# Kernel optimization log

Hardware: AMD Instinct MI355X
Metric: run time of the kernel (lower is better)

## Reference

```python
import jax, jax.numpy as jnp
import numpy as np

NB, H = 4, 8          # blocks, heads
B, S = 2, 1024        # batch, seq
D, HID = 512, 512     # input_dim, hidden_dim (must match, see zeros_like(x) branch)
# mod computed from neurochem BEFORE _modulate_neurochem, using init values
MOD = 0.5 * 1.1 + 0.5 * 0.7 + 0.5 * 1.3 - 0.0 * 1.2  # = 1.55


def setup_inputs() -> dict:
    key = jax.random.key(0)
    ks = jax.random.split(key, 12)
    sc = 1.0 / np.sqrt(D)
    inp = {
        "x": jax.random.normal(ks[0], (B, S, D), jnp.float32),
        "Wq": jax.random.normal(ks[1], (NB, D, HID), jnp.float32) * sc,
        "bq": jax.random.normal(ks[2], (NB, HID), jnp.float32) * sc,
        "Wk": jax.random.normal(ks[3], (NB, D, HID), jnp.float32) * sc,
        "bk": jax.random.normal(ks[4], (NB, HID), jnp.float32) * sc,
        "Wv": jax.random.normal(ks[5], (NB, D, HID), jnp.float32) * sc,
        "bv": jax.random.normal(ks[6], (NB, HID), jnp.float32) * sc,
        "Wo": jax.random.normal(ks[7], (NB, HID, D), jnp.float32) * sc,
        "bo": jax.random.normal(ks[8], (NB, D), jnp.float32) * sc,
        "strength": jax.random.uniform(ks[9], (NB, H, H), jnp.float32),
        # gate = (osc_mask * spike_mask > 0.5) materialized as 0/1 floats
        "gate": (jax.random.uniform(ks[10], (NB, H)) < 0.7).astype(jnp.float32),
    }
    return inp


def reference(x, Wq, bq, Wk, bk, Wv, bv, Wo, bo, strength, gate):
    # per-block projections (shared across heads in the original loop)
    q = jnp.einsum('bsd,ndh->nbsh', x, Wq) + bq[:, None, None, :]
    k = jnp.einsum('bsd,ndh->nbsh', x, Wk) + bk[:, None, None, :]
    v = jnp.einsum('bsd,ndh->nbsh', x, Wv) + bv[:, None, None, :]
    scores = jnp.einsum('nbsh,nbth->nbst', q, k) / jnp.sqrt(jnp.float32(HID))
    # per-head scalar bias: diagonal synaptic strength, clamped
    s = jnp.clip(jnp.diagonal(strength, axis1=1, axis2=2), 0.01, 1.0)  # [NB, H]
    scaled = scores[:, None] * s[:, :, None, None, None]  # [NB, H, B, S, S]
    probs = jax.nn.softmax(scaled, axis=-1)
    # head outputs summed with the 0/1 osc*spike gate
    head_sum = jnp.einsum('nhbst,nbtd,nh->nbsd', probs, v, gate)  # [NB, B, S, HID]
    block_out = jnp.einsum('nbsd,ndo->nbso', head_sum, Wo) + bo[:, None, None, :]
    return block_out.sum(axis=0) * jnp.float32(MOD)
```

## Files before the change

kernel.cpp:

```cpp
#include <hip/hip_runtime.h>
#include <math.h>

#define NBLK   4
#define NH     8
#define BATCH  2
#define SEQ    1024
#define DIM    512
#define HIDDEN 512
#define MODF   1.55f
#define INV_SQRT_HID 0.04419417382415922f

typedef __bf16 bf16;
typedef __bf16 bf16x4 __attribute__((ext_vector_type(4)));
typedef __bf16 bf16x8 __attribute__((ext_vector_type(8)));
typedef float  floatx4 __attribute__((ext_vector_type(4)));

constexpr int BM = 128, BN = 128, BK = 32;

__device__ __forceinline__ void load16_lds(const bf16* g, bf16* l) {
    __builtin_amdgcn_global_load_lds(
        (__attribute__((address_space(1))) void*)g,
        (__attribute__((address_space(3))) void*)l, 16, 0, 0);
}

__device__ __forceinline__ void stage32(
    const bf16* __restrict__ Ab, int lda,
    const bf16* __restrict__ Bb, int ldb, int k0,
    bf16* As, bf16* Bs, int w, int l)
{
    const int s0 = 2 * w, s1 = s0 + 1;
    const int r0 = s0 * 16 + (l >> 2);
    const int r1 = s1 * 16 + (l >> 2);
    const int kc = (l & 3) * 8;
    load16_lds(Ab + (size_t)r0 * lda + k0 + kc, As + s0 * 512);
    load16_lds(Ab + (size_t)r1 * lda + k0 + kc, As + s1 * 512);
    load16_lds(Bb + (size_t)r0 * ldb + k0 + kc, Bs + s0 * 512);
    load16_lds(Bb + (size_t)r1 * ldb + k0 + kc, Bs + s1 * 512);
}

__device__ __forceinline__ void comp32(
    const bf16* As, const bf16* Bs,
    int wr, int wc, int fr, int fk, floatx4 (&acc)[4][4])
{
    bf16x8 af[4], bg[4];
#pragma unroll
    for (int i = 0; i < 4; ++i)
        af[i] = *(const bf16x8*)&As[(wr + i * 16 + fr) * BK + fk];
#pragma unroll
    for (int j = 0; j < 4; ++j)
        bg[j] = *(const bf16x8*)&Bs[(wc + j * 16 + fr) * BK + fk];
#pragma unroll
    for (int i = 0; i < 4; ++i)
#pragma unroll
        for (int j = 0; j < 4; ++j)
            acc[i][j] = __builtin_amdgcn_mfma_f32_16x16x32_bf16(
                af[i], bg[j], acc[i][j], 0, 0, 0);
}

__device__ __forceinline__ void mfma_nt(
    const bf16* __restrict__ A, int lda,
    const bf16* __restrict__ B, int ldb,
    int K, int m0, int n0, floatx4 (&acc)[4][4])
{
    __shared__ __align__(16) bf16 As0[BM * BK];
    __shared__ __align__(16) bf16 Bs0[BN * BK];
    __shared__ __align__(16) bf16 As1[BM * BK];
    __shared__ __align__(16) bf16 Bs1[BN * BK];

    const int tid = threadIdx.x;
    const int l   = tid & 63;
    const int w   = tid >> 6;
    const int wr  = (w >> 1) * 64;
    const int wc  = (w & 1) * 64;
    const int fr  = l & 15;
    const int fk  = (l >> 4) * 8;

    const bf16* Ab = A + (size_t)m0 * lda;
    const bf16* Bb = B + (size_t)n0 * ldb;

    const int nIter = K / BK;
    stage32(Ab, lda, Bb, ldb, 0, As0, Bs0, w, l);
    for (int k = 0; k < nIter; k += 2) {
        __syncthreads();
        if (k + 1 < nIter)
            stage32(Ab, lda, Bb, ldb, (k + 1) * BK, As1, Bs1, w, l);
        comp32(As0, Bs0, wr, wc, fr, fk, acc);
        __syncthreads();
        if (k + 2 < nIter)
            stage32(Ab, lda, Bb, ldb, (k + 2) * BK, As0, Bs0, w, l);
        comp32(As1, Bs1, wr, wc, fr, fk, acc);
    }
}

__global__ __launch_bounds__(256) void xconv_kernel(
    const float* __restrict__ x, bf16* __restrict__ xb)
{
    const int t = blockIdx.x * 256 + threadIdx.x;
    const float4 v = ((const float4*)x)[t];
    bf16x4 o = { (bf16)v.x, (bf16)v.y, (bf16)v.z, (bf16)v.w };
    *(bf16x4*)&xb[(size_t)t * 4] = o;
}

__global__ __launch_bounds__(256) void transpose_w_kernel(
    const float* __restrict__ Wq, const float* __restrict__ Wk,
    const float* __restrict__ Wv, const float* __restrict__ Wo,
    bf16* __restrict__ WqT, bf16* __restrict__ WkT,
    bf16* __restrict__ WvT, bf16* __restrict__ WoT)
{
    __shared__ float tile[32][33];
    const int z = blockIdx.z;
    const int mat = z >> 2, n = z & 3;
    const float* src; bf16* dst;
    if (mat == 0)      { src = Wq; dst = WqT; }
    else if (mat == 1) { src = Wk; dst = WkT; }
    else if (mat == 2) { src = Wv; dst = WvT; }
    else               { src = Wo; dst = WoT; }
    src += (size_t)n * 512 * 512;
    dst += (size_t)n * 512 * 512;

    const int tx = threadIdx.x & 31, ty = threadIdx.x >> 5;
    const int x0 = blockIdx.x * 32, y0 = blockIdx.y * 32;
#pragma unroll
    for (int r = 0; r < 4; ++r)
        tile[ty + r * 8][tx] = src[(size_t)(y0 + ty + r * 8) * 512 + x0 + tx];
    __syncthreads();
#pragma unroll
    for (int r = 0; r < 4; ++r)
        dst[(size_t)(x0 + ty + r * 8) * 512 + y0 + tx] = (bf16)tile[tx][ty + r * 8];
}

__global__ __launch_bounds__(256) void proj_mfma_kernel(
    const bf16* __restrict__ xb,
    const bf16* __restrict__ WqT, const bf16* __restrict__ WkT,
    const bf16* __restrict__ WvT,
    const float* __restrict__ bq, const float* __restrict__ bk,
    const float* __restrict__ bv,
    bf16* __restrict__ Qh, bf16* __restrict__ Kh, bf16* __restrict__ Vt)
{
    const int z = blockIdx.z;
    const int n = z & 3, which = z >> 2;
    const bf16* WT; const float* bias;
    if (which == 0)      { WT = WqT; bias = bq; }
    else if (which == 1) { WT = WkT; bias = bk; }
    else                 { WT = WvT; bias = bv; }
    WT   += (size_t)n * DIM * HIDDEN;
    bias += (size_t)n * HIDDEN;

    const int m0 = blockIdx.y * BM, n0 = blockIdx.x * BN;
    floatx4 acc[4][4] = {};
    mfma_nt(xb, DIM, WT, DIM, DIM, m0, n0, acc);

    const int l = threadIdx.x & 63, w = threadIdx.x >> 6;
    const int rb = m0 + (w >> 1) * 64 + (l >> 4) * 4;
    const int cb = n0 + (w & 1) * 64 + (l & 15);

    if (which != 2) {
        bf16* C = (which ? Kh : Qh) + (size_t)n * (BATCH * SEQ) * HIDDEN;
#pragma unroll
        for (int j = 0; j < 4; ++j) {
            const int col = cb + j * 16;
            const float bc = bias[col];
#pragma unroll
            for (int i = 0; i < 4; ++i)
#pragma unroll
                for (int r = 0; r < 4; ++r)
                    C[(size_t)(rb + i * 16 + r) * HIDDEN + col] = (bf16)(acc[i][j][r] + bc);
        }
    } else {
        const int b = m0 >> 10;
        bf16* Cv = Vt + (size_t)(n * BATCH + b) * HIDDEN * SEQ;
        const int tb = rb & (SEQ - 1);
#pragma unroll
        for (int j = 0; j < 4; ++j) {
            const int col = cb + j * 16;
            const float bc = bias[col];
#pragma unroll
            for (int i = 0; i < 4; ++i) {
                bf16x4 o = { (bf16)(acc[i][j][0] + bc), (bf16)(acc[i][j][1] + bc),
                             (bf16)(acc[i][j][2] + bc), (bf16)(acc[i][j][3] + bc) };
                *(bf16x4*)&Cv[(size_t)col * SEQ + tb + i * 16] = o;
            }
        }
    }
}

__global__ __launch_bounds__(256) void scores_mfma_kernel(
    const bf16* __restrict__ Qh, const bf16* __restrict__ Kh,
    float* __restrict__ P)
{
    const int z = blockIdx.z;
    const bf16* A = Qh + (size_t)z * SEQ * HIDDEN;
    const bf16* B = Kh + (size_t)z * SEQ * HIDDEN;
    float* C = P + (size_t)z * SEQ * SEQ;

    const int m0 = blockIdx.y * BM, n0 = blockIdx.x * BN;
    floatx4 acc[4][4] = {};
    mfma_nt(A, HIDDEN, B, HIDDEN, HIDDEN, m0, n0, acc);

    const int l = threadIdx.x & 63, w = threadIdx.x >> 6;
    const int rb = m0 + (w >> 1) * 64 + (l >> 4) * 4;
    const int cb = n0 + (w & 1) * 64 + (l & 15);
#pragma unroll
    for (int i = 0; i < 4; ++i)
#pragma unroll
        for (int j = 0; j < 4; ++j)
#pragma unroll
            for (int r = 0; r < 4; ++r)
                C[(size_t)(rb + i * 16 + r) * SEQ + cb + j * 16] =
                    acc[i][j][r] * INV_SQRT_HID;
}

__global__ __launch_bounds__(256) void softmax_combine_kernel(
    const float* __restrict__ P, bf16* __restrict__ Pb,
    const float* __restrict__ strength, const float* __restrict__ gate)
{
    const int row = blockIdx.x;
    const int n = row >> 11;
    const float* prow = P + (size_t)row * SEQ;
    const int tid = threadIdx.x;
    const int wid = tid >> 6, lane = tid & 63;

    float4 v = ((const float4*)prow)[tid];

    float m = fmaxf(fmaxf(v.x, v.y), fmaxf(v.z, v.w));
#pragma unroll
    for (int off = 32; off > 0; off >>= 1) m = fmaxf(m, __shfl_down(m, off));
    __shared__ float redm[4];
    if (lane == 0) redm[wid] = m;
    __syncthreads();
    const float M = fmaxf(fmaxf(redm[0], redm[1]), fmaxf(redm[2], redm[3]));

    float sh[NH], gh[NH];
#pragma unroll
    for (int h = 0; h < NH; ++h) {
        sh[h] = fminf(fmaxf(strength[n * NH * NH + h * NH + h], 0.01f), 1.0f);
        gh[h] = gate[n * NH + h];
    }

    const float e[4] = { v.x - M, v.y - M, v.z - M, v.w - M };
    float E[4][NH];
    float zsum[NH];
#pragma unroll
    for (int h = 0; h < NH; ++h) zsum[h] = 0.f;
#pragma unroll
    for (int i = 0; i < 4; ++i)
#pragma unroll
        for (int h = 0; h < NH; ++h) {
            const float t = __expf(sh[h] * e[i]);
            E[i][h] = t; zsum[h] += t;
        }

#pragma unroll
    for (int h = 0; h < NH; ++h)
#pragma unroll
        for (int off = 32; off > 0; off >>= 1) zsum[h] += __shfl_down(zsum[h], off);
    __shared__ float redz[4][NH];
    if (lane == 0)
#pragma unroll
        for (int h = 0; h < NH; ++h) redz[wid][h] = zsum[h];
    __syncthreads();

    float wgt[NH];
#pragma unroll
    for (int h = 0; h < NH; ++h) {
        const float Z = redz[0][h] + redz[1][h] + redz[2][h] + redz[3][h];
        wgt[h] = gh[h] / Z;
    }

    bf16x4 o;
#pragma unroll
    for (int i = 0; i < 4; ++i) {
        float s = 0.f;
#pragma unroll
        for (int h = 0; h < NH; ++h) s += wgt[h] * E[i][h];
        o[i] = (bf16)s;
    }
    *(bf16x4*)&Pb[(size_t)row * SEQ + tid * 4] = o;
}

__global__ __launch_bounds__(256) void pv_mfma_kernel(
    const bf16* __restrict__ Pb, const bf16* __restrict__ Vt,
    bf16* __restrict__ HS)
{
    const int z = blockIdx.z;
    const bf16* A = Pb + (size_t)z * SEQ * SEQ;
    const bf16* B = Vt + (size_t)z * HIDDEN * SEQ;
    bf16* C = HS + (size_t)z * SEQ * HIDDEN;

    const int m0 = blockIdx.y * BM, n0 = blockIdx.x * BN;
    floatx4 acc[4][4] = {};
    mfma_nt(A, SEQ, B, SEQ, SEQ, m0, n0, acc);

    const int l = threadIdx.x & 63, w = threadIdx.x >> 6;
    const int rb = m0 + (w >> 1) * 64 + (l >> 4) * 4;
    const int cb = n0 + (w & 1) * 64 + (l & 15);
#pragma unroll
    for (int i = 0; i < 4; ++i)
#pragma unroll
        for (int j = 0; j < 4; ++j)
#pragma unroll
            for (int r = 0; r < 4; ++r)
                C[(size_t)(rb + i * 16 + r) * HIDDEN + cb + j * 16] =
                    (bf16)acc[i][j][r];
}

__global__ __launch_bounds__(256) void out_partial_kernel(
    const bf16* __restrict__ HS, const bf16* __restrict__ WoT,
    float* __restrict__ Opart)
{
    const int n = blockIdx.z;
    const bf16* A = HS + (size_t)n * (BATCH * SEQ) * HIDDEN;
    const bf16* B = WoT + (size_t)n * HIDDEN * DIM;
    float* C = Opart + (size_t)n * (BATCH * SEQ) * DIM;

    const int m0 = blockIdx.y * BM, n0 = blockIdx.x * BN;
    floatx4 acc[4][4] = {};
    mfma_nt(A, HIDDEN, B, HIDDEN, HIDDEN, m0, n0, acc);

    const int l = threadIdx.x & 63, w = threadIdx.x >> 6;
    const int rb = m0 + (w >> 1) * 64 + (l >> 4) * 4;
    const int cb = n0 + (w & 1) * 64 + (l & 15);
#pragma unroll
    for (int i = 0; i < 4; ++i)
#pragma unroll
        for (int j = 0; j < 4; ++j)
#pragma unroll
            for (int r = 0; r < 4; ++r)
                C[(size_t)(rb + i * 16 + r) * DIM + cb + j * 16] = acc[i][j][r];
}

__global__ __launch_bounds__(256) void out_reduce_kernel(
    const float* __restrict__ Opart, const float* __restrict__ bo,
    float* __restrict__ out)
{
    const size_t t = (size_t)blockIdx.x * 256 + threadIdx.x;
    const int c = (int)((t * 4) & (DIM - 1));
    const size_t stride4 = (size_t)(BATCH * SEQ) * DIM / 4;

    float4 s = ((const float4*)Opart)[t];
#pragma unroll
    for (int n = 1; n < NBLK; ++n) {
        const float4 p = ((const float4*)Opart)[t + n * stride4];
        s.x += p.x; s.y += p.y; s.z += p.z; s.w += p.w;
    }
    float4 bs = make_float4(0.f, 0.f, 0.f, 0.f);
#pragma unroll
    for (int n = 0; n < NBLK; ++n) {
        const float4 b = *(const float4*)(bo + n * DIM + c);
        bs.x += b.x; bs.y += b.y; bs.z += b.z; bs.w += b.w;
    }
    ((float4*)out)[t] = make_float4((s.x + bs.x) * MODF, (s.y + bs.y) * MODF,
                                    (s.z + bs.z) * MODF, (s.w + bs.w) * MODF);
}

extern "C" void kernel_launch(void* const* d_in, const int* in_sizes, int n_in,
                              void* d_out, int out_size, void* d_ws, size_t ws_size,
                              hipStream_t stream) {
    const float* x        = (const float*)d_in[0];
    const float* Wq       = (const float*)d_in[1];
    const float* bq       = (const float*)d_in[2];
    const float* Wk       = (const float*)d_in[3];
    const float* bk       = (const float*)d_in[4];
    const float* Wv       = (const float*)d_in[5];
    const float* bv       = (const float*)d_in[6];
    const float* Wo       = (const float*)d_in[7];
    const float* bo       = (const float*)d_in[8];
    const float* strength = (const float*)d_in[9];
    const float* gate     = (const float*)d_in[10];
    float* out = (float*)d_out;

    char* ws = (char*)d_ws;
    bf16*  xb    = (bf16*)(ws);
    bf16*  WqT   = (bf16*)(ws + (2u  << 20));
    bf16*  WkT   = (bf16*)(ws + (4u  << 20));
    bf16*  WvT   = (bf16*)(ws + (6u  << 20));
    bf16*  WoT   = (bf16*)(ws + (8u  << 20));
    bf16*  Qh    = (bf16*)(ws + (10u << 20));
    bf16*  Kh    = (bf16*)(ws + (18u << 20));
    bf16*  Vt    = (bf16*)(ws + (26u << 20));
    float* Pf    = (float*)(ws + (34u << 20));
    bf16*  Pb    = (bf16*)(ws + (10u << 20));
    bf16*  HS    = (bf16*)(ws + (34u << 20));
    float* Opart = (float*)(ws + (42u << 20));

    xconv_kernel<<<dim3((BATCH * SEQ * DIM) / 1024), 256, 0, stream>>>(x, xb);
    transpose_w_kernel<<<dim3(16, 16, 16), 256, 0, stream>>>(
        Wq, Wk, Wv, Wo, WqT, WkT, WvT, WoT);

    proj_mfma_kernel<<<dim3(HIDDEN / BN, (BATCH * SEQ) / BM, 3 * NBLK), 256, 0, stream>>>(
        xb, WqT, WkT, WvT, bq, bk, bv, Qh, Kh, Vt);

    scores_mfma_kernel<<<dim3(SEQ / BN, SEQ / BM, NBLK * BATCH), 256, 0, stream>>>(
        Qh, Kh, Pf);

    softmax_combine_kernel<<<dim3(NBLK * BATCH * SEQ), 256, 0, stream>>>(
        Pf, Pb, strength, gate);

    pv_mfma_kernel<<<dim3(HIDDEN / BN, SEQ / BM, NBLK * BATCH), 256, 0, stream>>>(
        Pb, Vt, HS);

    out_partial_kernel<<<dim3(DIM / BN, (BATCH * SEQ) / BM, NBLK), 256, 0, stream>>>(
        HS, WoT, Opart);

    out_reduce_kernel<<<dim3((BATCH * SEQ) * DIM / 4 / 256), 256, 0, stream>>>(
        Opart, bo, out);
}
```

Baseline: 194.2 us.

## Switch GEMMs to 32x32x16 MFMA and use deeper K tiles

Replaces the 16x16x32 bf16 MFMA tiles with 32x32x16 MFMA instructions (2x2 per wave instead of 4x4) and templatizes the K tile depth, using BK=64 for scores, PV and output GEMMs. Fewer LDS fragment loads per FLOP and fewer barriers per K step are the intended savings. The epilogues are rewritten for the 32x32 accumulator layout. Doubling LDS per block may reduce occupancy, and LDS bank conflicts with the 64-wide rows are possible.

Result: slower. 211.6 us (+9.0%).

```diff
diff --git a/kernel.cpp b/kernel.cpp
--- a/kernel.cpp
+++ b/kernel.cpp
@@ -13,9 +13,10 @@
 typedef __bf16 bf16;
 typedef __bf16 bf16x4 __attribute__((ext_vector_type(4)));
 typedef __bf16 bf16x8 __attribute__((ext_vector_type(8)));
-typedef float  floatx4 __attribute__((ext_vector_type(4)));
-
-constexpr int BM = 128, BN = 128, BK = 32;
+typedef float  floatx4  __attribute__((ext_vector_type(4)));
+typedef float  floatx16 __attribute__((ext_vector_type(16)));
+
+constexpr int BM = 128, BN = 128;
 
 __device__ __forceinline__ void load16_lds(const bf16* g, bf16* l) {
     __builtin_amdgcn_global_load_lds(
@@ -23,72 +24,83 @@
         (__attribute__((address_space(3))) void*)l, 16, 0, 0);
 }
 
-__device__ __forceinline__ void stage32(
+template<int BKT>
+__device__ __forceinline__ void stageT(
     const bf16* __restrict__ Ab, int lda,
     const bf16* __restrict__ Bb, int ldb, int k0,
     bf16* As, bf16* Bs, int w, int l)
 {
-    const int s0 = 2 * w, s1 = s0 + 1;
-    const int r0 = s0 * 16 + (l >> 2);
-    const int r1 = s1 * 16 + (l >> 2);
-    const int kc = (l & 3) * 8;
-    load16_lds(Ab + (size_t)r0 * lda + k0 + kc, As + s0 * 512);
-    load16_lds(Ab + (size_t)r1 * lda + k0 + kc, As + s1 * 512);
-    load16_lds(Bb + (size_t)r0 * ldb + k0 + kc, Bs + s0 * 512);
-    load16_lds(Bb + (size_t)r1 * ldb + k0 + kc, Bs + s1 * 512);
-}
-
-__device__ __forceinline__ void comp32(
+    constexpr int NL  = BKT / 16;
+    constexpr int RPS = 512 / BKT;
+    constexpr int CPL = BKT / 8;
+#pragma unroll
+    for (int i = 0; i < NL; ++i) {
+        const int seg = w * NL + i;
+        const int row = seg * RPS + l / CPL;
+        const int kc  = (l % CPL) * 8;
+        load16_lds(Ab + (size_t)row * lda + k0 + kc, As + seg * 512);
+    }
+#pragma unroll
+    for (int i = 0; i < NL; ++i) {
+        const int seg = w * NL + i;
+        const int row = seg * RPS + l / CPL;
+        const int kc  = (l % CPL) * 8;
+        load16_lds(Bb + (size_t)row * ldb + k0 + kc, Bs + seg * 512);
+    }
+}
+
+template<int BKT>
+__device__ __forceinline__ void compT(
     const bf16* As, const bf16* Bs,
-    int wr, int wc, int fr, int fk, floatx4 (&acc)[4][4])
-{
-    bf16x8 af[4], bg[4];
-#pragma unroll
-    for (int i = 0; i < 4; ++i)
-        af[i] = *(const bf16x8*)&As[(wr + i * 16 + fr) * BK + fk];
-#pragma unroll
-    for (int j = 0; j < 4; ++j)
-        bg[j] = *(const bf16x8*)&Bs[(wc + j * 16 + fr) * BK + fk];
-#pragma unroll
-    for (int i = 0; i < 4; ++i)
-#pragma unroll
-        for (int j = 0; j < 4; ++j)
-            acc[i][j] = __builtin_amdgcn_mfma_f32_16x16x32_bf16(
-                af[i], bg[j], acc[i][j], 0, 0, 0);
-}
-
+    int wr, int wc, int l, floatx16 (&acc)[2][2])
+{
+    const int fr = l & 31;
+    const int fk = (l >> 5) * 8;
+#pragma unroll
+    for (int ks = 0; ks < BKT / 16; ++ks) {
+        const int ko = ks * 16 + fk;
+        const bf16x8 a0 = *(const bf16x8*)&As[(wr + fr)      * BKT + ko];
+        const bf16x8 a1 = *(const bf16x8*)&As[(wr + 32 + fr) * BKT + ko];
+        const bf16x8 b0 = *(const bf16x8*)&Bs[(wc + fr)      * BKT + ko];
+        const bf16x8 b1 = *(const bf16x8*)&Bs[(wc + 32 + fr) * BKT + ko];
+        acc[0][0] = __builtin_amdgcn_mfma_f32_32x32x16_bf16(a0, b0, acc[0][0], 0, 0, 0);
+        acc[0][1] = __builtin_amdgcn_mfma_f32_32x32x16_bf16(a0, b1, acc[0][1], 0, 0, 0);
+        acc[1][0] = __builtin_amdgcn_mfma_f32_32x32x16_bf16(a1, b0, acc[1][0], 0, 0, 0);
+        acc[1][1] = __builtin_amdgcn_mfma_f32_32x32x16_bf16(a1, b1, acc[1][1], 0, 0, 0);
+    }
+}
+
+template<int BKT>
 __device__ __forceinline__ void mfma_nt(
     const bf16* __restrict__ A, int lda,
     const bf16* __restrict__ B, int ldb,
-    int K, int m0, int n0, floatx4 (&acc)[4][4])
-{
-    __shared__ __align__(16) bf16 As0[BM * BK];
-    __shared__ __align__(16) bf16 Bs0[BN * BK];
-    __shared__ __align__(16) bf16 As1[BM * BK];
-    __shared__ __align__(16) bf16 Bs1[BN * BK];
+    int K, int m0, int n0, floatx16 (&acc)[2][2])
+{
+    __shared__ __align__(16) bf16 As0[BM * BKT];
+    __shared__ __align__(16) bf16 Bs0[BN * BKT];
+    __shared__ __align__(16) bf16 As1[BM * BKT];
+    __shared__ __align__(16) bf16 Bs1[BN * BKT];
 
     const int tid = threadIdx.x;
     const int l   = tid & 63;
     const int w   = tid >> 6;
     const int wr  = (w >> 1) * 64;
     const int wc  = (w & 1) * 64;
-    const int fr  = l & 15;
-    const int fk  = (l >> 4) * 8;
 
     const bf16* Ab = A + (size_t)m0 * lda;
     const bf16* Bb = B + (size_t)n0 * ldb;
 
-    const int nIter = K / BK;
-    stage32(Ab, lda, Bb, ldb, 0, As0, Bs0, w, l);
+    const int nIter = K / BKT;
+    stageT<BKT>(Ab, lda, Bb, ldb, 0, As0, Bs0, w, l);
     for (int k = 0; k < nIter; k += 2) {
         __syncthreads();
         if (k + 1 < nIter)
-            stage32(Ab, lda, Bb, ldb, (k + 1) * BK, As1, Bs1, w, l);
-        comp32(As0, Bs0, wr, wc, fr, fk, acc);
+            stageT<BKT>(Ab, lda, Bb, ldb, (k + 1) * BKT, As1, Bs1, w, l);
+        compT<BKT>(As0, Bs0, wr, wc, l, acc);
         __syncthreads();
         if (k + 2 < nIter)
-            stage32(Ab, lda, Bb, ldb, (k + 2) * BK, As0, Bs0, w, l);
-        comp32(As1, Bs1, wr, wc, fr, fk, acc);
+            stageT<BKT>(Ab, lda, Bb, ldb, (k + 2) * BKT, As0, Bs0, w, l);
+        compT<BKT>(As1, Bs1, wr, wc, l, acc);
     }
 }
 
@@ -147,38 +159,47 @@
     bias += (size_t)n * HIDDEN;
 
     const int m0 = blockIdx.y * BM, n0 = blockIdx.x * BN;
-    floatx4 acc[4][4] = {};
-    mfma_nt(xb, DIM, WT, DIM, DIM, m0, n0, acc);
+    floatx16 acc[2][2] = {};
+    mfma_nt<32>(xb, DIM, WT, DIM, DIM, m0, n0, acc);
 
     const int l = threadIdx.x & 63, w = threadIdx.x >> 6;
-    const int rb = m0 + (w >> 1) * 64 + (l >> 4) * 4;
-    const int cb = n0 + (w & 1) * 64 + (l & 15);
+    const int fr = l & 31, hs = (l >> 5) * 4;
+    const int wr = (w >> 1) * 64, wc = (w & 1) * 64;
 
     if (which != 2) {
         bf16* C = (which ? Kh : Qh) + (size_t)n * (BATCH * SEQ) * HIDDEN;
 #pragma unroll
-        for (int j = 0; j < 4; ++j) {
-            const int col = cb + j * 16;
+        for (int j = 0; j < 2; ++j) {
+            const int col = n0 + wc + j * 32 + fr;
             const float bc = bias[col];
 #pragma unroll
-            for (int i = 0; i < 4; ++i)
-#pragma unroll
-                for (int r = 0; r < 4; ++r)
-                    C[(size_t)(rb + i * 16 + r) * HIDDEN + col] = (bf16)(acc[i][j][r] + bc);
+            for (int i = 0; i < 2; ++i) {
+                const int rb2 = m0 + wr + i * 32 + hs;
+#pragma unroll
+                for (int r = 0; r < 16; ++r) {
+                    const int row = rb2 + (r & 3) + 8 * (r >> 2);
+                    C[(size_t)row * HIDDEN + col] = (bf16)(acc[i][j][r] + bc);
+                }
+            }
         }
     } else {
         const int b = m0 >> 10;
         bf16* Cv = Vt + (size_t)(n * BATCH + b) * HIDDEN * SEQ;
-        const int tb = rb & (SEQ - 1);
-#pragma unroll
-        for (int j = 0; j < 4; ++j) {
-            const int col = cb + j * 16;
+#pragma unroll
+        for (int j = 0; j < 2; ++j) {
+            const int col = n0 + wc + j * 32 + fr;
             const float bc = bias[col];
 #pragma unroll
-            for (int i = 0; i < 4; ++i) {
-                bf16x4 o = { (bf16)(acc[i][j][0] + bc), (bf16)(acc[i][j][1] + bc),
-                             (bf16)(acc[i][j][2] + bc), (bf16)(acc[i][j][3] + bc) };
-                *(bf16x4*)&Cv[(size_t)col * SEQ + tb + i * 16] = o;
+            for (int i = 0; i < 2; ++i) {
+                const int tb2 = (m0 + wr + i * 32 + hs) & (SEQ - 1);
+#pragma unroll
+                for (int g = 0; g < 4; ++g) {
+                    bf16x4 o = { (bf16)(acc[i][j][4 * g + 0] + bc),
+                                 (bf16)(acc[i][j][4 * g + 1] + bc),
+                                 (bf16)(acc[i][j][4 * g + 2] + bc),
+                                 (bf16)(acc[i][j][4 * g + 3] + bc) };
+                    *(bf16x4*)&Cv[(size_t)col * SEQ + tb2 + 8 * g] = o;
+                }
             }
         }
     }
@@ -194,20 +215,25 @@
     float* C = P + (size_t)z * SEQ * SEQ;
 
     const int m0 = blockIdx.y * BM, n0 = blockIdx.x * BN;
-    floatx4 acc[4][4] = {};
-    mfma_nt(A, HIDDEN, B, HIDDEN, HIDDEN, m0, n0, acc);
+    floatx16 acc[2][2] = {};
+    mfma_nt<64>(A, HIDDEN, B, HIDDEN, HIDDEN, m0, n0, acc);
 
     const int l = threadIdx.x & 63, w = threadIdx.x >> 6;
-    const int rb = m0 + (w >> 1) * 64 + (l >> 4) * 4;
-    const int cb = n0 + (w & 1) * 64 + (l & 15);
-#pragma unroll
-    for (int i = 0; i < 4; ++i)
-#pragma unroll
-        for (int j = 0; j < 4; ++j)
-#pragma unroll
-            for (int r = 0; r < 4; ++r)
-                C[(size_t)(rb + i * 16 + r) * SEQ + cb + j * 16] =
-                    acc[i][j][r] * INV_SQRT_HID;
+    const int fr = l & 31, hs = (l >> 5) * 4;
+    const int wr = (w >> 1) * 64, wc = (w & 1) * 64;
+#pragma unroll
+    for (int i = 0; i < 2; ++i) {
+        const int rb2 = m0 + wr + i * 32 + hs;
+#pragma unroll
+        for (int j = 0; j < 2; ++j) {
+            const int col = n0 + wc + j * 32 + fr;
+#pragma unroll
+            for (int r = 0; r < 16; ++r) {
+                const int row = rb2 + (r & 3) + 8 * (r >> 2);
+                C[(size_t)row * SEQ + col] = acc[i][j][r] * INV_SQRT_HID;
+            }
+        }
+    }
 }
 
 __global__ __launch_bounds__(256) void softmax_combine_kernel(
@@ -288,20 +314,25 @@
     bf16* C = HS + (size_t)z * SEQ * HIDDEN;
 
     const int m0 = blockIdx.y * BM, n0 = blockIdx.x * BN;
-    floatx4 acc[4][4] = {};
-    mfma_nt(A, SEQ, B, SEQ, SEQ, m0, n0, acc);
+    floatx16 acc[2][2] = {};
+    mfma_nt<64>(A, SEQ, B, SEQ, SEQ, m0, n0, acc);
 
     const int l = threadIdx.x & 63, w = threadIdx.x >> 6;
-    const int rb = m0 + (w >> 1) * 64 + (l >> 4) * 4;
-    const int cb = n0 + (w & 1) * 64 + (l & 15);
-#pragma unroll
-    for (int i = 0; i < 4; ++i)
-#pragma unroll
-        for (int j = 0; j < 4; ++j)
-#pragma unroll
-            for (int r = 0; r < 4; ++r)
-                C[(size_t)(rb + i * 16 + r) * HIDDEN + cb + j * 16] =
-                    (bf16)acc[i][j][r];
+    const int fr = l & 31, hs = (l >> 5) * 4;
+    const int wr = (w >> 1) * 64, wc = (w & 1) * 64;
+#pragma unroll
+    for (int i = 0; i < 2; ++i) {
+        const int rb2 = m0 + wr + i * 32 + hs;
+#pragma unroll
+        for (int j = 0; j < 2; ++j) {
+            const int col = n0 + wc + j * 32 + fr;
+#pragma unroll
+            for (int r = 0; r < 16; ++r) {
+                const int row = rb2 + (r & 3) + 8 * (r >> 2);
+                C[(size_t)row * HIDDEN + col] = (bf16)acc[i][j][r];
+            }
+        }
+    }
 }
 
 __global__ __launch_bounds__(256) void out_partial_kernel(
@@ -314,19 +345,25 @@
     float* C = Opart + (size_t)n * (BATCH * SEQ) * DIM;
 
     const int m0 = blockIdx.y * BM, n0 = blockIdx.x * BN;
-    floatx4 acc[4][4] = {};
-    mfma_nt(A, HIDDEN, B, HIDDEN, HIDDEN, m0, n0, acc);
+    floatx16 acc[2][2] = {};
+    mfma_nt<64>(A, HIDDEN, B, HIDDEN, HIDDEN, m0, n0, acc);
 
     const int l = threadIdx.x & 63, w = threadIdx.x >> 6;
-    const int rb = m0 + (w >> 1) * 64 + (l >> 4) * 4;
-    const int cb = n0 + (w & 1) * 64 + (l & 15);
-#pragma unroll
-    for (int i = 0; i < 4; ++i)
-#pragma unroll
-        for (int j = 0; j < 4; ++j)
-#pragma unroll
-            for (int r = 0; r < 4; ++r)
-                C[(size_t)(rb + i * 16 + r) * DIM + cb + j * 16] = acc[i][j][r];
+    const int fr = l & 31, hs = (l >> 5) * 4;
+    const int wr = (w >> 1) * 64, wc = (w & 1) * 64;
+#pragma unroll
+    for (int i = 0; i < 2; ++i) {
+        const int rb2 = m0 + wr + i * 32 + hs;
+#pragma unroll
+        for (int j = 0; j < 2; ++j) {
+            const int col = n0 + wc + j * 32 + fr;
+#pragma unroll
+            for (int r = 0; r < 16; ++r) {
+                const int row = rb2 + (r & 3) + 8 * (r >> 2);
+                C[(size_t)row * DIM + col] = acc[i][j][r];
+            }
+        }
+    }
 }
 
 __global__ __launch_bounds__(256) void out_reduce_kernel(
```
